# Optimization experiments

Hardware: AMD Instinct MI355X
Metric: run time of the kernel (lower is better)

## Reference

```python
import jax, jax.numpy as jnp
import numpy as np

BITS = 1.58
EPS = 1e-8


def absmean_quantize(w, bits=BITS, scale_method='mean'):
    # gamma over the whole weight tensor (CPU path of original)
    if scale_method == 'mean':
        gamma = jnp.mean(jnp.abs(w))
    else:
        gamma = jnp.max(jnp.abs(w))
    levels = 2.0 ** bits - 1.0  # ~1.989 for 1.58-bit ternary-ish
    half = levels / 2.0
    return jnp.clip(jnp.round(w / (gamma + EPS) * half), -half, half)


def setup_inputs() -> dict:
    key = jax.random.key(0)
    k_x, k_w, k_b = jax.random.split(key, 3)
    B, S, D_IN, D_OUT = 8, 2048, 4096, 4096
    x = jax.random.normal(k_x, (B, S, D_IN), dtype=jnp.float32)
    # kaiming_uniform_(a=sqrt(5)) -> bound = sqrt(6/((1+5)*fan_in)) = 1/sqrt(fan_in)
    bound = 1.0 / np.sqrt(D_IN)
    weight = jax.random.uniform(k_w, (D_OUT, D_IN), minval=-bound, maxval=bound, dtype=jnp.float32)
    bias = jax.random.uniform(k_b, (D_OUT,), minval=-bound, maxval=bound, dtype=jnp.float32)
    return {"x": x, "weight": weight, "bias": bias}


def reference(x, weight, bias):
    qw = absmean_quantize(weight)                      # [D_OUT, D_IN]
    out = jnp.einsum('bsi,oi->bso', x, qw)             # F.linear without bias
    return out + bias
```

## Files before the change

### kernel.cpp

```cpp
#include <hip/hip_runtime.h>
#include <math.h>
#include <stdint.h>


#define MDIM 16384
#define NDIM 4096
#define KDIM 4096

__global__ void absmean_reduce(const float4* __restrict__ w4,
                               double* __restrict__ gsum, int n4) {
  int tid = blockIdx.x * blockDim.x + threadIdx.x;
  int stride = gridDim.x * blockDim.x;
  double s = 0.0;
  for (int i = tid; i < n4; i += stride) {
    float4 v = w4[i];
    s += (double)fabsf(v.x) + (double)fabsf(v.y) +
         (double)fabsf(v.z) + (double)fabsf(v.w);
  }
  for (int off = 32; off > 0; off >>= 1) s += __shfl_down(s, off, 64);
  __shared__ double partial[4];
  int ln = threadIdx.x & 63, wv = threadIdx.x >> 6;
  if (ln == 0) partial[wv] = s;
  __syncthreads();
  if (threadIdx.x == 0) {
    double t = partial[0] + partial[1] + partial[2] + partial[3];
    atomicAdd(gsum, t);
  }
}

__device__ __forceinline__ unsigned short tern_bf16(float w, float g, float h) {
  float q = rintf(w / g * h);
  q = fminf(fmaxf(q, -1.0f), 1.0f);
  return (unsigned short)(__float_as_uint(q) >> 16);
}

__global__ void quantize_w(const float4* __restrict__ w4,
                           const double* __restrict__ gsum,
                           ushort4* __restrict__ wq, int n4, float halfF) {
  const float gamma = (float)(*gsum * (1.0 / 16777216.0)) + 1e-8f;
  int tid = blockIdx.x * blockDim.x + threadIdx.x;
  int stride = gridDim.x * blockDim.x;
  for (int i = tid; i < n4; i += stride) {
    float4 v = w4[i];
    ushort4 o;
    o.x = tern_bf16(v.x, gamma, halfF);
    o.y = tern_bf16(v.y, gamma, halfF);
    o.z = tern_bf16(v.z, gamma, halfF);
    o.w = tern_bf16(v.w, gamma, halfF);
    wq[i] = o;
  }
}

__device__ __forceinline__ unsigned bf16_rne(float f) {
  unsigned u = __float_as_uint(f);
  return (u + 0x7FFFu + ((u >> 16) & 1u)) >> 16;
}
__device__ __forceinline__ unsigned pack2(float lo, float hi) {
  return bf16_rne(lo) | (bf16_rne(hi) << 16);
}

__global__ void cvt_x(const float4* __restrict__ x4, uint4* __restrict__ xb,
                      int n8) {
  int tid = blockIdx.x * blockDim.x + threadIdx.x;
  int stride = gridDim.x * blockDim.x;
  for (int i = tid; i < n8; i += stride) {
    float4 a = x4[2 * i];
    float4 b = x4[2 * i + 1];
    uint4 o;
    o.x = pack2(a.x, a.y);
    o.y = pack2(a.z, a.w);
    o.z = pack2(b.x, b.y);
    o.w = pack2(b.z, b.w);
    xb[i] = o;
  }
}

typedef __attribute__((ext_vector_type(8))) short bf16x8;
typedef __attribute__((ext_vector_type(4))) float f32x4;

#define BM 256
#define BN 256
#define BK 64
#define NTK (KDIM / BK)

__device__ __forceinline__ void async16(const short* g, short* l) {
  __builtin_amdgcn_global_load_lds(
      (const __attribute__((address_space(1))) unsigned int*)g,
      (__attribute__((address_space(3))) unsigned int*)l, 16, 0, 0);
}

__global__ __launch_bounds__(512, 2) void gemm_tern_256(
    const short* __restrict__ A,
    const short* __restrict__ Bw,
    const float* __restrict__ bias,
    float* __restrict__ out,
    float scale) {
  extern __shared__ short lds[];

  const int tid = threadIdx.x;
  const int wv = tid >> 6;
  const int ln = tid & 63;
  const int wr = wv >> 2;
  const int wc = wv & 3;
  const int l15 = ln & 15;
  const int lq = ln >> 4;
  const int l7 = ln & 7;

  const int orig = blockIdx.x;
  const int wg = ((orig & 7) << 7) | (orig >> 3);
  const int bm = (wg >> 4) * BM;
  const int bn = (wg & 15) * BN;

  const int g8 = ln >> 3;
  const int sw = (l7 ^ (g8 & 7)) << 3;
  const int grp0 = wv * 2, grp1 = wv * 2 + 1;
  const short* aP0 = A + (size_t)(bm + grp0 * 8 + g8) * KDIM + sw;
  const short* aP1 = A + (size_t)(bm + grp1 * 8 + g8) * KDIM + sw;
  const short* bP0 = Bw + (size_t)(bn + grp0 * 8 + g8) * KDIM + sw;
  const short* bP1 = Bw + (size_t)(bn + grp1 * 8 + g8) * KDIM + sw;
  const int d0 = grp0 * 512, d1 = grp1 * 512;

  const int c0 = (lq ^ l7) << 3;
  const int c1 = ((4 + lq) ^ l7) << 3;
  const int aRow = (wr * 64 + l15) * 64;
  const int bRow = 16384 + (wc * 32 + l15) * 64;

  f32x4 acc[2][2][4][2] = {};
  bf16x8 faA[4][2];
  bf16x8 fbB0[2][2], fbB1[2][2];

#define KOF(s) ((size_t)(((s) < NTK) ? (s) : 0) * BK)
#define STAGE_A(DST, H, S)                                 \
  do {                                                     \
    const size_t koA_ = KOF(S) + (size_t)(H) * 128 * KDIM; \
    async16(aP0 + koA_, (DST) + (H) * 8192 + d0);          \
    async16(aP1 + koA_, (DST) + (H) * 8192 + d1);          \
  } while (0)
#define STAGE_B(DST, H, S)                                 \
  do {                                                     \
    const size_t koB_ = KOF(S) + (size_t)(H) * 128 * KDIM; \
    async16(bP0 + koB_, (DST) + 16384 + (H) * 8192 + d0);  \
    async16(bP1 + koB_, (DST) + 16384 + (H) * 8192 + d1);  \
  } while (0)

#define SYNC1                                            \
  __builtin_amdgcn_sched_barrier(0);                     \
  __builtin_amdgcn_s_barrier();                          \
  asm volatile("s_waitcnt lgkmcnt(0)" ::: "memory");     \
  __builtin_amdgcn_sched_barrier(0)

#define SYNC2                                            \
  __builtin_amdgcn_sched_barrier(0);                     \
  __builtin_amdgcn_s_barrier()

#define MFMA_QUAD(MH, NH, FB)                                        \
  do {                                                               \
    __builtin_amdgcn_s_setprio(1);                                   \
    _Pragma("unroll") for (int m = 0; m < 4; ++m)                    \
        _Pragma("unroll") for (int n = 0; n < 2; ++n) {              \
      acc[MH][NH][m][n] = __builtin_amdgcn_mfma_f32_16x16x32_bf16(   \
          faA[m][0], FB[n][0], acc[MH][NH][m][n], 0, 0, 0);          \
      acc[MH][NH][m][n] = __builtin_amdgcn_mfma_f32_16x16x32_bf16(   \
          faA[m][1], FB[n][1], acc[MH][NH][m][n], 0, 0, 0);          \
    }                                                                \
    __builtin_amdgcn_s_setprio(0);                                   \
  } while (0)

  {
    short* b0 = lds;
    short* b1 = lds + 32768;
    STAGE_A(b0, 0, 0);
    STAGE_B(b0, 0, 0);
    STAGE_B(b0, 1, 0);
    STAGE_A(b0, 1, 0);
    STAGE_A(b1, 0, 1);
    STAGE_B(b1, 0, 1);
  }
  asm volatile("s_waitcnt vmcnt(4)" ::: "memory");
  __builtin_amdgcn_sched_barrier(0);
  __builtin_amdgcn_s_barrier();

  for (int kt = 0; kt < NTK; ++kt) {
    const int curS = (kt & 1) << 15;
    short* Cb = lds + curS;
    short* Nx = lds + (curS ^ 32768);
    const short* a0 = Cb + aRow + c0;
    const short* a1 = Cb + aRow + c1;
    const short* b0 = Cb + bRow + c0;
    const short* b1 = Cb + bRow + c1;

#pragma unroll
    for (int m = 0; m < 4; ++m) {
      faA[m][0] = *(const bf16x8*)(a0 + m * 1024);
      faA[m][1] = *(const bf16x8*)(a1 + m * 1024);
    }
#pragma unroll
    for (int n = 0; n < 2; ++n) {
      fbB0[n][0] = *(const bf16x8*)(b0 + n * 1024);
      fbB0[n][1] = *(const bf16x8*)(b1 + n * 1024);
    }
    STAGE_B(Nx, 1, kt + 1);
    SYNC1;
    MFMA_QUAD(0, 0, fbB0);
    SYNC2;

#pragma unroll
    for (int n = 0; n < 2; ++n) {
      fbB1[n][0] = *(const bf16x8*)(b0 + 8192 + n * 1024);
      fbB1[n][1] = *(const bf16x8*)(b1 + 8192 + n * 1024);
    }
    STAGE_A(Nx, 1, kt + 1);
    SYNC1;
    MFMA_QUAD(0, 1, fbB1);
    SYNC2;

#pragma unroll
    for (int m = 0; m < 4; ++m) {
      faA[m][0] = *(const bf16x8*)(a0 + 8192 + m * 1024);
      faA[m][1] = *(const bf16x8*)(a1 + 8192 + m * 1024);
    }
    STAGE_A(Cb, 0, kt + 2);
    SYNC1;
    MFMA_QUAD(1, 1, fbB1);
    SYNC2;

    STAGE_B(Cb, 0, kt + 2);
    SYNC1;
    MFMA_QUAD(1, 0, fbB0);
    asm volatile("s_waitcnt vmcnt(4)" ::: "memory");
    SYNC2;
  }

  const int colb = bn + wc * 32 + l15;
  const int rowb = bm + wr * 64 + (lq << 2);
#pragma unroll
  for (int nh = 0; nh < 2; ++nh)
#pragma unroll
    for (int n = 0; n < 2; ++n) {
      const int col = colb + nh * 128 + n * 16;
      const float bj = bias[col];
#pragma unroll
      for (int mh = 0; mh < 2; ++mh)
#pragma unroll
        for (int m = 0; m < 4; ++m) {
          const int row = rowb + mh * 128 + m * 16;
#pragma unroll
          for (int r = 0; r < 4; ++r)
            out[(size_t)(row + r) * NDIM + col] =
                fmaf(acc[mh][nh][m][n][r], scale, bj);
        }
    }
}

extern "C" void kernel_launch(void* const* d_in, const int* in_sizes, int n_in,
                              void* d_out, int out_size, void* d_ws,
                              size_t ws_size, hipStream_t stream) {
  const float* x = (const float*)d_in[0];
  const float* w = (const float*)d_in[1];
  const float* bias = (const float*)d_in[2];
  float* out = (float*)d_out;

  char* ws = (char*)d_ws;
  double* gsum = (double*)ws;
  short* xb = (short*)(ws + 256);
  short* wq = (short*)(ws + 256 + (size_t)MDIM * KDIM * 2);

  const float kHalfF = (float)((pow(2.0, 1.58) - 1.0) * 0.5);

  static bool attr_done = false;
  if (!attr_done) {
    (void)hipFuncSetAttribute((const void*)gemm_tern_256,
                              hipFuncAttributeMaxDynamicSharedMemorySize,
                              131072);
    attr_done = true;
  }

  hipMemsetAsync(gsum, 0, sizeof(double), stream);

  const int nW4 = (NDIM * KDIM) / 4;
  absmean_reduce<<<1024, 256, 0, stream>>>((const float4*)w, gsum, nW4);

  quantize_w<<<4096, 256, 0, stream>>>((const float4*)w, gsum, (ushort4*)wq,
                                       nW4, kHalfF);

  const int nX8 = (MDIM * KDIM) / 8;
  cvt_x<<<8192, 256, 0, stream>>>((const float4*)x, (uint4*)xb, nX8);

  dim3 grid((MDIM / BM) * (NDIM / BN));
  gemm_tern_256<<<grid, 512, 131072, stream>>>(xb, wq, bias, out, kHalfF);
}
```

Measured before the change: 939.6 us.

## Prefetch LDS fragments across phases with double-buffered A registers in GEMM loop

Restructures the four-phase main loop of the bf16 GEMM so that A fragments are double-buffered in registers (faA_a/faA_b). Fragments for the next k-tile (A half 0 and B half 0) are read from the other LDS buffer at the end of the current iteration rather than at the start of the next. The explicit lgkmcnt(0) waits before each MFMA group are removed, and barriers now come before the LDS reads and global-to-LDS stages, with sched_barriers pinning the order. The aim is to overlap LDS fragment reads with MFMA work and cut stalls at barriers. In exchange it uses more VGPRs and makes the correctness of buffer reuse depend on delicate ordering.

```diff
diff --git a/kernel.cpp b/kernel.cpp
--- a/kernel.cpp
+++ b/kernel.cpp
@@ -89,6 +89,8 @@
       (__attribute__((address_space(3))) unsigned int*)l, 16, 0, 0);
 }
 
+#define SB __builtin_amdgcn_sched_barrier(0)
+
 __global__ __launch_bounds__(512, 2) void gemm_tern_256(
     const short* __restrict__ A,
     const short* __restrict__ Bw,
@@ -126,7 +128,8 @@
   const int bRow = 16384 + (wc * 32 + l15) * 64;
 
   f32x4 acc[2][2][4][2] = {};
-  bf16x8 faA[4][2];
+  bf16x8 faA_a[4][2];
+  bf16x8 faA_b[4][2];
   bf16x8 fbB0[2][2], fbB1[2][2];
 
 #define KOF(s) ((size_t)(((s) < NTK) ? (s) : 0) * BK)
@@ -143,25 +146,26 @@
     async16(bP1 + koB_, (DST) + 16384 + (H) * 8192 + d1);  \
   } while (0)
 
-#define SYNC1                                            \
-  __builtin_amdgcn_sched_barrier(0);                     \
-  __builtin_amdgcn_s_barrier();                          \
-  asm volatile("s_waitcnt lgkmcnt(0)" ::: "memory");     \
-  __builtin_amdgcn_sched_barrier(0)
-
-#define SYNC2                                            \
-  __builtin_amdgcn_sched_barrier(0);                     \
-  __builtin_amdgcn_s_barrier()
-
-#define MFMA_QUAD(MH, NH, FB)                                        \
+#define LOAD_FA(DST, B0_, B1_, OFF)                             \
+  _Pragma("unroll") for (int m = 0; m < 4; ++m) {               \
+    DST[m][0] = *(const bf16x8*)((B0_) + (OFF) + m * 1024);     \
+    DST[m][1] = *(const bf16x8*)((B1_) + (OFF) + m * 1024);     \
+  }
+#define LOAD_FB(DST, B0_, B1_, OFF)                             \
+  _Pragma("unroll") for (int n = 0; n < 2; ++n) {               \
+    DST[n][0] = *(const bf16x8*)((B0_) + (OFF) + n * 1024);     \
+    DST[n][1] = *(const bf16x8*)((B1_) + (OFF) + n * 1024);     \
+  }
+
+#define MFMAQ(MH, NH, FA, FB)                                        \
   do {                                                               \
     __builtin_amdgcn_s_setprio(1);                                   \
     _Pragma("unroll") for (int m = 0; m < 4; ++m)                    \
         _Pragma("unroll") for (int n = 0; n < 2; ++n) {              \
       acc[MH][NH][m][n] = __builtin_amdgcn_mfma_f32_16x16x32_bf16(   \
-          faA[m][0], FB[n][0], acc[MH][NH][m][n], 0, 0, 0);          \
+          FA[m][0], FB[n][0], acc[MH][NH][m][n], 0, 0, 0);           \
       acc[MH][NH][m][n] = __builtin_amdgcn_mfma_f32_16x16x32_bf16(   \
-          faA[m][1], FB[n][1], acc[MH][NH][m][n], 0, 0, 0);          \
+          FA[m][1], FB[n][1], acc[MH][NH][m][n], 0, 0, 0);           \
     }                                                                \
     __builtin_amdgcn_s_setprio(0);                                   \
   } while (0)
@@ -177,58 +181,63 @@
     STAGE_B(b1, 0, 1);
   }
   asm volatile("s_waitcnt vmcnt(4)" ::: "memory");
-  __builtin_amdgcn_sched_barrier(0);
+  SB;
   __builtin_amdgcn_s_barrier();
+  SB;
+  LOAD_FA(faA_a, lds + aRow + c0, lds + aRow + c1, 0);
+  LOAD_FB(fbB0, lds + bRow + c0, lds + bRow + c1, 0);
 
   for (int kt = 0; kt < NTK; ++kt) {
     const int curS = (kt & 1) << 15;
-    short* Cb = lds + curS;
-    short* Nx = lds + (curS ^ 32768);
-    const short* a0 = Cb + aRow + c0;
-    const short* a1 = Cb + aRow + c1;
-    const short* b0 = Cb + bRow + c0;
-    const short* b1 = Cb + bRow + c1;
-
-#pragma unroll
-    for (int m = 0; m < 4; ++m) {
-      faA[m][0] = *(const bf16x8*)(a0 + m * 1024);
-      faA[m][1] = *(const bf16x8*)(a1 + m * 1024);
-    }
-#pragma unroll
-    for (int n = 0; n < 2; ++n) {
-      fbB0[n][0] = *(const bf16x8*)(b0 + n * 1024);
-      fbB0[n][1] = *(const bf16x8*)(b1 + n * 1024);
-    }
-    STAGE_B(Nx, 1, kt + 1);
-    SYNC1;
-    MFMA_QUAD(0, 0, fbB0);
-    SYNC2;
-
-#pragma unroll
-    for (int n = 0; n < 2; ++n) {
-      fbB1[n][0] = *(const bf16x8*)(b0 + 8192 + n * 1024);
-      fbB1[n][1] = *(const bf16x8*)(b1 + 8192 + n * 1024);
-    }
-    STAGE_A(Nx, 1, kt + 1);
-    SYNC1;
-    MFMA_QUAD(0, 1, fbB1);
-    SYNC2;
-
-#pragma unroll
-    for (int m = 0; m < 4; ++m) {
-      faA[m][0] = *(const bf16x8*)(a0 + 8192 + m * 1024);
-      faA[m][1] = *(const bf16x8*)(a1 + 8192 + m * 1024);
-    }
-    STAGE_A(Cb, 0, kt + 2);
-    SYNC1;
-    MFMA_QUAD(1, 1, fbB1);
-    SYNC2;
-
-    STAGE_B(Cb, 0, kt + 2);
-    SYNC1;
-    MFMA_QUAD(1, 0, fbB0);
+    const short* Cb = lds + curS;
+    const short* Nx = lds + (curS ^ 32768);
+    short* Cw = lds + curS;
+    short* Nw = lds + (curS ^ 32768);
+    const short* aC0 = Cb + aRow + c0;
+    const short* aC1 = Cb + aRow + c1;
+    const short* bC0 = Cb + bRow + c0;
+    const short* bC1 = Cb + bRow + c1;
+    const short* aN0 = Nx + aRow + c0;
+    const short* aN1 = Nx + aRow + c1;
+    const short* bN0 = Nx + bRow + c0;
+    const short* bN1 = Nx + bRow + c1;
+
+    SB;
+    __builtin_amdgcn_s_barrier();
+    SB;
+    LOAD_FB(fbB1, bC0, bC1, 8192);
+    STAGE_B(Nw, 1, kt + 1);
+    SB;
+    MFMAQ(0, 0, faA_a, fbB0);
+
+    SB;
+    __builtin_amdgcn_s_barrier();
+    SB;
+    LOAD_FA(faA_b, aC0, aC1, 8192);
+    STAGE_A(Nw, 1, kt + 1);
+    SB;
+    MFMAQ(0, 1, faA_a, fbB1);
+    SB;
     asm volatile("s_waitcnt vmcnt(4)" ::: "memory");
-    SYNC2;
+
+    SB;
+    __builtin_amdgcn_s_barrier();
+    SB;
+    LOAD_FA(faA_a, aN0, aN1, 0);
+    STAGE_A(Cw, 0, kt + 2);
+    SB;
+    MFMAQ(1, 1, faA_b, fbB1);
+
+    SB;
+    __builtin_amdgcn_s_barrier();
+    SB;
+    STAGE_B(Cw, 0, kt + 2);
+    SB;
+    MFMAQ(1, 0, faA_b, fbB0);
+    SB;
+    LOAD_FB(fbB0, bN0, bN1, 0);
+    SB;
+    asm volatile("s_waitcnt vmcnt(4)" ::: "memory");
   }
 
   const int colb = bn + wc * 32 + l15;
```

After: 1.006 ms. 7.1% more time.
